# Kernel optimization log

Hardware: AMD Instinct MI355X
Metric: run time of the kernel (lower is better)

Reference implementation:

```python
import jax, jax.numpy as jnp
import numpy as np


def setup_inputs() -> dict:
    key = jax.random.key(0)
    ks = jax.random.split(key, 6)
    B, N, F, H, E = 2, 50000, 64, 32, 800000
    x = jax.random.normal(ks[0], (B, N, F), dtype=jnp.float32)
    edge_index = jax.random.randint(ks[1], (2, E), 0, N, dtype=jnp.int64)
    h_cur = jax.random.normal(ks[2], (B, N, H), dtype=jnp.float32)
    c_cur = jax.random.normal(ks[3], (B, N, H), dtype=jnp.float32)
    W = jax.random.normal(ks[4], (F + H, 4 * H), dtype=jnp.float32) * (1.0 / np.sqrt(F + H))
    b = jax.random.normal(ks[5], (4 * H,), dtype=jnp.float32) * 0.01
    return {"x": x, "edge_index": edge_index, "h_cur": h_cur, "c_cur": c_cur, "W": W, "b": b}


def reference(x, edge_index, h_cur, c_cur, W, b):
    B, N, _ = x.shape
    H = h_cur.shape[-1]

    # --- GCNConv on concatenated [x, h] ---
    combined = jnp.concatenate([x, h_cur], axis=-1)          # [B, N, F+H]
    xw = jnp.einsum('bnf,fg->bng', combined, W)              # [B, N, 4H]

    # add self-loops
    loop = jnp.arange(N, dtype=edge_index.dtype)
    src = jnp.concatenate([edge_index[0], loop])             # [E+N]
    dst = jnp.concatenate([edge_index[1], loop])             # [E+N]

    # symmetric degree normalization: deg over target index (PyG gcn_norm)
    deg = jnp.zeros((N,), dtype=xw.dtype).at[dst].add(1.0)
    dinv = jnp.where(deg > 0, jax.lax.rsqrt(deg), 0.0)
    norm = dinv[src] * dinv[dst]                             # [E+N]

    # gather-scale-scatter aggregation
    msgs = xw[:, src, :] * norm[None, :, None]               # [B, E+N, 4H]
    agg = jnp.zeros((B, N, 4 * H), dtype=xw.dtype).at[:, dst, :].add(msgs)
    conv = agg + b                                           # [B, N, 4H]

    # --- LSTM gating ---
    cc_i, cc_f, cc_o, cc_g = jnp.split(conv, 4, axis=-1)
    i = jax.nn.sigmoid(cc_i)
    f = jax.nn.sigmoid(cc_f)
    o = jax.nn.sigmoid(cc_o)
    g = jnp.tanh(cc_g)
    c_next = f * c_cur + i * g
    h_next = o * jnp.tanh(c_next)
    return h_next, c_next
```

## Files before the change

### kernel.cpp

```cpp
#include <hip/hip_runtime.h>
#include <hip/hip_bf16.h>

constexpr int H_DIM = 32;
constexpr int KPAD  = 104;
constexpr int CAP   = 64;

typedef __attribute__((ext_vector_type(8))) short bf16x8;
typedef __attribute__((ext_vector_type(4))) float f32x4;

static __device__ __forceinline__ unsigned short f2bf_bits(float v) {
    __hip_bfloat16 b = __float2bfloat16(v);
    return *reinterpret_cast<unsigned short*>(&b);
}
static __device__ __forceinline__ unsigned pack2(float a, float b) {
    return (unsigned)f2bf_bits(a) | ((unsigned)f2bf_bits(b) << 16);
}
static __device__ __forceinline__ float lo_f(unsigned u) { return __uint_as_float(u << 16); }
static __device__ __forceinline__ float hi_f(unsigned u) { return __uint_as_float(u & 0xffff0000u); }

static __device__ __forceinline__ void fma4p(const uint4 u, float d, float* a)
{
    a[0] = fmaf(lo_f(u.x), d, a[0]);
    a[4] = fmaf(hi_f(u.x), d, a[4]);
    a[1] = fmaf(lo_f(u.y), d, a[1]);
    a[5] = fmaf(hi_f(u.y), d, a[5]);
    a[2] = fmaf(lo_f(u.z), d, a[2]);
    a[6] = fmaf(hi_f(u.z), d, a[6]);
    a[3] = fmaf(lo_f(u.w), d, a[3]);
    a[7] = fmaf(hi_f(u.w), d, a[7]);
}

__global__ __launch_bounds__(256)
void prep_kernel(const float* __restrict__ W,
                 unsigned short* __restrict__ Wt,
                 unsigned* __restrict__ cnt, int N)
{
    int gt = blockIdx.x * 256 + threadIdx.x;
    if (gt < N) cnt[gt] = 0u;
    if (gt < 96 * 128) {
        int k = gt >> 7;
        int n = gt & 127;
        Wt[n * 96 + k] = f2bf_bits(W[gt]);
    }
}

__global__ __launch_bounds__(256)
void fill_convert_kernel(const float* __restrict__ x,
                         const float* __restrict__ h,
                         const int* __restrict__ ei,
                         unsigned* __restrict__ cnt,
                         unsigned short* __restrict__ bucket,
                         unsigned* __restrict__ z,
                         int N, int E, int fillGrid)
{
    const int bi = blockIdx.x;
    if (bi < fillGrid) {
        int e = bi * 256 + threadIdx.x;
        if (e < E) {
            int dst = ei[E + e];
            unsigned pos = atomicAdd(&cnt[dst], 1u);
            if (pos < CAP) bucket[(long)dst * CAP + pos] = (unsigned short)ei[e];
        }
        return;
    }
    long idx = (long)(bi - fillGrid) * 256 + threadIdx.x;
    if (idx >= (long)N * 24) return;
    int n  = (int)(idx / 24);
    int ku = (int)(idx - (long)n * 24);
    int f0 = 4 * ku;
    float4 a, b;
    if (f0 < 64) {
        a = *reinterpret_cast<const float4*>(x + (long)n * 64 + f0);
        b = *reinterpret_cast<const float4*>(x + ((long)N + n) * 64 + f0);
    } else {
        a = *reinterpret_cast<const float4*>(h + (long)n * 32 + (f0 - 64));
        b = *reinterpret_cast<const float4*>(h + ((long)N + n) * 32 + (f0 - 64));
    }
    uint4 o;
    o.x = pack2(a.x, b.x);
    o.y = pack2(a.y, b.y);
    o.z = pack2(a.z, b.z);
    o.w = pack2(a.w, b.w);
    *reinterpret_cast<uint4*>(z + idx * 4) = o;
}

__global__ __launch_bounds__(256)
void gather_kernel(const unsigned* __restrict__ cnt,
                   const unsigned short* __restrict__ bucket,
                   const unsigned* __restrict__ z,
                   unsigned* __restrict__ aggz, int N)
{
    const int wid  = (int)(((long)blockIdx.x * 256 + threadIdx.x) >> 6);
    const int lane = threadIdx.x & 63;
    const int g    = lane >> 5;
    const int w    = lane & 31;
    const bool live = (wid < N);
    const int n = live ? wid : 0;

    const int dn = live ? min((int)cnt[n], CAP) : 0;
    const unsigned short* __restrict__ brow = bucket + (long)n * CAP;
    const unsigned* __restrict__ zw = z + 4 * w;

    float acc[8];
    #pragma unroll
    for (int j = 0; j < 8; ++j) acc[j] = 0.f;

    for (int base = 0; base < dn; base += 64) {
        int cnt64 = min(64, dn - base);
        int   s_reg = 0;
        float d_reg = 0.f;
        if (lane < cnt64) {
            s_reg = (int)brow[base + lane];
            d_reg = rsqrtf((float)cnt[s_reg] + 1.f);
        }
        for (int i = 0; i < cnt64; i += 8) {
            int i0 = i + g, i1 = i + 2 + g, i2 = i + 4 + g, i3 = i + 6 + g;
            int   s0 = __shfl(s_reg, i0);  float d0 = __shfl(d_reg, i0);
            int   s1 = __shfl(s_reg, i1);  float d1 = __shfl(d_reg, i1);
            int   s2 = __shfl(s_reg, i2);  float d2 = __shfl(d_reg, i2);
            int   s3 = __shfl(s_reg, i3);  float d3 = __shfl(d_reg, i3);
            if (i0 >= cnt64) d0 = 0.f;
            if (i1 >= cnt64) d1 = 0.f;
            if (i2 >= cnt64) d2 = 0.f;
            if (i3 >= cnt64) d3 = 0.f;
            uint4 u0 = make_uint4(0,0,0,0), u1 = u0, u2 = u0, u3 = u0;
            if (w < 24) {
                u0 = *reinterpret_cast<const uint4*>(zw + (long)s0 * 96);
                u1 = *reinterpret_cast<const uint4*>(zw + (long)s1 * 96);
                u2 = *reinterpret_cast<const uint4*>(zw + (long)s2 * 96);
                u3 = *reinterpret_cast<const uint4*>(zw + (long)s3 * 96);
            }
            fma4p(u0, d0, acc);
            fma4p(u1, d1, acc);
            fma4p(u2, d2, acc);
            fma4p(u3, d3, acc);
        }
    }

    #pragma unroll
    for (int j = 0; j < 8; ++j) acc[j] += __shfl_xor(acc[j], 32);

    if (live && g == 0 && w < 24) {
        float di  = rsqrtf((float)cnt[n] + 1.f);
        float di2 = di * di;
        uint4 us = *reinterpret_cast<const uint4*>(zw + (long)n * 96);
        uint4 o;
        o.x = pack2(fmaf(di, acc[0], di2 * lo_f(us.x)), fmaf(di, acc[4], di2 * hi_f(us.x)));
        o.y = pack2(fmaf(di, acc[1], di2 * lo_f(us.y)), fmaf(di, acc[5], di2 * hi_f(us.y)));
        o.z = pack2(fmaf(di, acc[2], di2 * lo_f(us.z)), fmaf(di, acc[6], di2 * hi_f(us.z)));
        o.w = pack2(fmaf(di, acc[3], di2 * lo_f(us.w)), fmaf(di, acc[7], di2 * hi_f(us.w)));
        *reinterpret_cast<uint4*>(aggz + (long)n * 96 + 4 * w) = o;
    }
}

__global__ __launch_bounds__(256)
void gemm_gates_kernel(const unsigned* __restrict__ aggz,
                       const unsigned short* __restrict__ Wt,
                       const float* __restrict__ bias,
                       const float* __restrict__ c_cur,
                       float* __restrict__ out,
                       int N)
{
    __shared__ __align__(16) unsigned short As[64 * KPAD];
    const int t  = threadIdx.x;
    const int n0 = blockIdx.x * 32;

    #pragma unroll
    for (int j = 0; j < 3; ++j) {
        int idx = t + 256 * j;
        int i   = idx / 24;
        int ku  = idx - 24 * i;
        int n   = n0 + i;
        uint4 u = make_uint4(0,0,0,0);
        if (n < N) u = *reinterpret_cast<const uint4*>(aggz + (long)n * 96 + 4 * ku);
        ushort4 lo, hi;
        lo.x = (unsigned short)u.x;  hi.x = (unsigned short)(u.x >> 16);
        lo.y = (unsigned short)u.y;  hi.y = (unsigned short)(u.y >> 16);
        lo.z = (unsigned short)u.z;  hi.z = (unsigned short)(u.z >> 16);
        lo.w = (unsigned short)u.w;  hi.w = (unsigned short)(u.w >> 16);
        *reinterpret_cast<ushort4*>(&As[i * KPAD + 4 * ku])        = lo;
        *reinterpret_cast<ushort4*>(&As[(32 + i) * KPAD + 4 * ku]) = hi;
    }
    __syncthreads();

    const int wv   = t >> 6;
    const int lane = t & 63;
    const int m    = lane & 15;
    const int q    = lane >> 4;

    f32x4 acc[8] = {};
    #pragma unroll
    for (int k0 = 0; k0 < 96; k0 += 32) {
        bf16x8 a = *reinterpret_cast<const bf16x8*>(&As[(wv * 16 + m) * KPAD + k0 + q * 8]);
        #pragma unroll
        for (int nt = 0; nt < 8; ++nt) {
            bf16x8 b = *reinterpret_cast<const bf16x8*>(&Wt[(nt * 16 + m) * 96 + k0 + q * 8]);
            acc[nt] = __builtin_amdgcn_mfma_f32_16x16x32_bf16(a, b, acc[nt], 0, 0, 0);
        }
    }

    const float bi0 = bias[m],       bi1 = bias[16 + m];
    const float bf0 = bias[32 + m],  bf1 = bias[48 + m];
    const float bo0 = bias[64 + m],  bo1 = bias[80 + m];
    const float bg0 = bias[96 + m],  bg1 = bias[112 + m];
    const long  co  = (long)2 * N * H_DIM;

    #pragma unroll
    for (int r = 0; r < 4; ++r) {
        int rr = wv * 16 + q * 4 + r;
        int b  = rr >> 5;
        int i  = rr & 31;
        int n  = n0 + i;
        if (n < N) {
            long base = ((long)b * N + n) * H_DIM;
            float c0 = c_cur[base + m];
            float c1 = c_cur[base + 16 + m];
            float ig0 = 1.f / (1.f + __expf(-(acc[0][r] + bi0)));
            float ig1 = 1.f / (1.f + __expf(-(acc[1][r] + bi1)));
            float fg0 = 1.f / (1.f + __expf(-(acc[2][r] + bf0)));
            float fg1 = 1.f / (1.f + __expf(-(acc[3][r] + bf1)));
            float og0 = 1.f / (1.f + __expf(-(acc[4][r] + bo0)));
            float og1 = 1.f / (1.f + __expf(-(acc[5][r] + bo1)));
            float gg0 = tanhf(acc[6][r] + bg0);
            float gg1 = tanhf(acc[7][r] + bg1);
            float cn0 = fmaf(fg0, c0, ig0 * gg0);
            float cn1 = fmaf(fg1, c1, ig1 * gg1);
            out[base + m]           = og0 * tanhf(cn0);
            out[base + 16 + m]      = og1 * tanhf(cn1);
            out[co + base + m]      = cn0;
            out[co + base + 16 + m] = cn1;
        }
    }
}

extern "C" void kernel_launch(void* const* d_in, const int* in_sizes, int n_in,
                              void* d_out, int out_size, void* d_ws, size_t ws_size,
                              hipStream_t stream)
{
    const float* x    = (const float*)d_in[0];
    const int*   ei   = (const int*)d_in[1];
    const float* h    = (const float*)d_in[2];
    const float* c    = (const float*)d_in[3];
    const float* W    = (const float*)d_in[4];
    const float* bias = (const float*)d_in[5];

    const int  E  = in_sizes[1] / 2;
    const long BN = (long)in_sizes[2] / H_DIM;
    const int  N  = (int)(BN / 2);

    char* ws = (char*)d_ws;
    unsigned* z = (unsigned*)ws;
    size_t off = (size_t)N * 96 * sizeof(unsigned);
    unsigned* aggz = (unsigned*)(ws + off);  off += (size_t)N * 96 * sizeof(unsigned);
    unsigned* cnt  = (unsigned*)(ws + off);  off += (size_t)N * sizeof(unsigned);
    unsigned short* bucket = (unsigned short*)(ws + off); off += (size_t)N * CAP * sizeof(unsigned short);
    unsigned short* Wt = (unsigned short*)(ws + off);     off += 96 * 128 * sizeof(unsigned short);

    int prep_grid = (max(N, 96 * 128) + 255) / 256;
    prep_kernel<<<prep_grid, 256, 0, stream>>>(W, Wt, cnt, N);

    int fillGrid = (E + 255) / 256;
    int convGrid = (int)(((long)N * 24 + 255) / 256);
    fill_convert_kernel<<<fillGrid + convGrid, 256, 0, stream>>>(
        x, h, ei, cnt, bucket, z, N, E, fillGrid);

    int gGrid = (int)(((long)N * 64 + 255) / 256);
    gather_kernel<<<gGrid, 256, 0, stream>>>(cnt, bucket, z, aggz, N);

    int mGrid = (N + 31) / 32;
    gemm_gates_kernel<<<mGrid, 256, 0, stream>>>(aggz, Wt, bias, c, (float*)d_out, N);
}
```

Before: 209.1 us.

## Build CSR buckets via two-pass partition by destination block instead of global atomics

Replaces the per-edge global atomicAdd bucket fill with a two-level scheme. Edges are first partitioned into 256-node destination blocks using shared-memory histograms and one global atomic per block per partition. A new kernel then builds each block's per-node buckets in LDS and writes them out with coalesced stores. The aim is to remove scattered global atomics and random 2-byte writes, at the cost of an extra kernel launch and an intermediate partition buffer with a fixed capacity (PCAP) that could overflow on skewed graphs.

```diff
diff --git a/kernel.cpp b/kernel.cpp
--- a/kernel.cpp
+++ b/kernel.cpp
@@ -4,6 +4,8 @@
 constexpr int H_DIM = 32;
 constexpr int KPAD  = 104;
 constexpr int CAP   = 64;
+constexpr int PCAP  = 5120;
+constexpr int EPB   = 2048;
 
 typedef __attribute__((ext_vector_type(8))) short bf16x8;
 typedef __attribute__((ext_vector_type(4))) float f32x4;
@@ -33,10 +35,10 @@
 __global__ __launch_bounds__(256)
 void prep_kernel(const float* __restrict__ W,
                  unsigned short* __restrict__ Wt,
-                 unsigned* __restrict__ cnt, int N)
+                 unsigned* __restrict__ pcnt)
 {
     int gt = blockIdx.x * 256 + threadIdx.x;
-    if (gt < N) cnt[gt] = 0u;
+    if (gt < 256) pcnt[gt] = 0u;
     if (gt < 96 * 128) {
         int k = gt >> 7;
         int n = gt & 127;
@@ -45,25 +47,54 @@
 }
 
 __global__ __launch_bounds__(256)
-void fill_convert_kernel(const float* __restrict__ x,
+void part_convert_kernel(const float* __restrict__ x,
                          const float* __restrict__ h,
                          const int* __restrict__ ei,
-                         unsigned* __restrict__ cnt,
-                         unsigned short* __restrict__ bucket,
+                         unsigned* __restrict__ pcnt,
+                         unsigned* __restrict__ part_buf,
                          unsigned* __restrict__ z,
-                         int N, int E, int fillGrid)
+                         int N, int E, int partGrid)
 {
     const int bi = blockIdx.x;
-    if (bi < fillGrid) {
-        int e = bi * 256 + threadIdx.x;
-        if (e < E) {
-            int dst = ei[E + e];
-            unsigned pos = atomicAdd(&cnt[dst], 1u);
-            if (pos < CAP) bucket[(long)dst * CAP + pos] = (unsigned short)ei[e];
+    if (bi < partGrid) {
+        __shared__ unsigned hist[256], basep[256], loff[256];
+        const int t = threadIdx.x;
+        hist[t] = 0u;
+        loff[t] = 0u;
+        __syncthreads();
+
+        unsigned pk[8];
+        const int e0 = bi * EPB + t;
+        #pragma unroll
+        for (int j = 0; j < 8; ++j) {
+            int e = e0 + 256 * j;
+            unsigned u = 0xFFFFFFFFu;
+            if (e < E) {
+                int src = ei[e];
+                int dst = ei[E + e];
+                int p   = dst >> 8;
+                u = (unsigned)src | ((unsigned)(dst & 255) << 16) | ((unsigned)p << 24);
+                atomicAdd(&hist[p], 1u);
+            }
+            pk[j] = u;
+        }
+        __syncthreads();
+        if (hist[t]) basep[t] = atomicAdd(&pcnt[t], hist[t]);
+        __syncthreads();
+        #pragma unroll
+        for (int j = 0; j < 8; ++j) {
+            unsigned u = pk[j];
+            if (u != 0xFFFFFFFFu) {
+                int p = (int)(u >> 24);
+                unsigned l = atomicAdd(&loff[p], 1u);
+                unsigned slot = basep[p] + l;
+                if (slot < PCAP) part_buf[(long)p * PCAP + slot] = u & 0x00FFFFFFu;
+            }
         }
         return;
     }
-    long idx = (long)(bi - fillGrid) * 256 + threadIdx.x;
+
+    long idx = (long)(bi - partGrid) * 256 + threadIdx.x;
     if (idx >= (long)N * 24) return;
     int n  = (int)(idx / 24);
     int ku = (int)(idx - (long)n * 24);
@@ -82,6 +113,43 @@
     o.z = pack2(a.z, b.z);
     o.w = pack2(a.w, b.w);
     *reinterpret_cast<uint4*>(z + idx * 4) = o;
+}
+
+__global__ __launch_bounds__(256)
+void bucket_build_kernel(const unsigned* __restrict__ pcnt,
+                         const unsigned* __restrict__ part_buf,
+                         unsigned* __restrict__ cnt,
+                         unsigned short* __restrict__ bucket,
+                         int N)
+{
+    __shared__ unsigned lcnt[256];
+    __shared__ __align__(16) unsigned short lbuck[256 * CAP];
+    const int p = blockIdx.x;
+    const int t = threadIdx.x;
+    lcnt[t] = 0u;
+    __syncthreads();
+
+    const int cp = (int)min(pcnt[p], (unsigned)PCAP);
+    const unsigned* __restrict__ pb = part_buf + (long)p * PCAP;
+    for (int i = t; i < cp; i += 256) {
+        unsigned u = pb[i];
+        int dl = (int)((u >> 16) & 0xFFu);
+        unsigned pos = atomicAdd(&lcnt[dl], 1u);
+        if (pos < CAP) lbuck[dl * CAP + pos] = (unsigned short)(u & 0xFFFFu);
+    }
+    __syncthreads();
+
+    int n = p * 256 + t;
+    if (n < N) cnt[n] = lcnt[t];
+    #pragma unroll
+    for (int j = 0; j < 8; ++j) {
+        int idx = t + 256 * j;
+        int row = idx >> 3, c = idx & 7;
+        int nn = p * 256 + row;
+        if (nn < N)
+            *reinterpret_cast<uint4*>(bucket + (long)nn * CAP + 8 * c) =
+                *reinterpret_cast<const uint4*>(&lbuck[row * CAP + 8 * c]);
+    }
 }
 
 __global__ __launch_bounds__(256)
@@ -247,6 +315,7 @@
     const int  E  = in_sizes[1] / 2;
     const long BN = (long)in_sizes[2] / H_DIM;
     const int  N  = (int)(BN / 2);
+    const int  NP = (N + 255) >> 8;
 
     char* ws = (char*)d_ws;
     unsigned* z = (unsigned*)ws;
@@ -255,14 +324,19 @@
     unsigned* cnt  = (unsigned*)(ws + off);  off += (size_t)N * sizeof(unsigned);
     unsigned short* bucket = (unsigned short*)(ws + off); off += (size_t)N * CAP * sizeof(unsigned short);
     unsigned short* Wt = (unsigned short*)(ws + off);     off += 96 * 128 * sizeof(unsigned short);
-
-    int prep_grid = (max(N, 96 * 128) + 255) / 256;
-    prep_kernel<<<prep_grid, 256, 0, stream>>>(W, Wt, cnt, N);
-
-    int fillGrid = (E + 255) / 256;
+    off = (off + 255) & ~(size_t)255;
+    unsigned* pcnt = (unsigned*)(ws + off);  off += 256 * sizeof(unsigned);
+    unsigned* part_buf = (unsigned*)(ws + off); off += (size_t)NP * PCAP * sizeof(unsigned);
+
+    int prep_grid = (96 * 128 + 255) / 256;
+    prep_kernel<<<prep_grid, 256, 0, stream>>>(W, Wt, pcnt);
+
+    int partGrid = (E + EPB - 1) / EPB;
     int convGrid = (int)(((long)N * 24 + 255) / 256);
-    fill_convert_kernel<<<fillGrid + convGrid, 256, 0, stream>>>(
-        x, h, ei, cnt, bucket, z, N, E, fillGrid);
+    part_convert_kernel<<<partGrid + convGrid, 256, 0, stream>>>(
+        x, h, ei, pcnt, part_buf, z, N, E, partGrid);
+
+    bucket_build_kernel<<<NP, 256, 0, stream>>>(pcnt, part_buf, cnt, bucket, N);
 
     int gGrid = (int)(((long)N * 64 + 255) / 256);
     gather_kernel<<<gGrid, 256, 0, stream>>>(cnt, bucket, z, aggz, N);
```

Result: faster. 187.6 us (-10.3%).
